# Kernel optimization log

Measured on AMD Instinct MI355X. Metric: run time of the kernel, lower is better.

## Reference

```python
import jax, jax.numpy as jnp
import numpy as np

# FlowNetC correlation config (kernel_size=1 -> pointwise patch; pad == max_displacement)
PAD = 20
MAX_DISP = 20
STRIDE2 = 2


def setup_inputs() -> dict:
    key = jax.random.key(0)
    k1, k2 = jax.random.split(key)
    B, C, H, W = 4, 256, 96, 96
    input1 = jax.random.normal(k1, (B, C, H, W), dtype=jnp.float32)
    input2 = jax.random.normal(k2, (B, C, H, W), dtype=jnp.float32)
    return {"input1": input1, "input2": input2}


def _correlation(x1, x2):
    # x1, x2: [B, C, H, W]. Output: [B, D*D, H, W] with D = 2*MAX_DISP//STRIDE2 + 1.
    B, C, H, W = x1.shape
    x2p = jnp.pad(x2, ((0, 0), (0, 0), (PAD, PAD), (PAD, PAD)))
    D = 2 * MAX_DISP // STRIDE2 + 1  # 21
    # start index into padded map = PAD + (disp) where disp = off - MAX_DISP;
    # since PAD == MAX_DISP, start index == off.
    offs = jnp.arange(D, dtype=jnp.int32) * STRIDE2
    dyv, dxv = jnp.meshgrid(offs, offs, indexing="ij")
    pairs = jnp.stack([dyv.ravel(), dxv.ravel()], axis=1)  # [D*D, 2]
    inv_c = jnp.float32(1.0 / C)  # CUDA kernel divides by kernel^2 * C (kernel=1)

    def body(_, p):
        dy, dx = p[0], p[1]
        sl = jax.lax.dynamic_slice(x2p, (0, 0, dy, dx), (B, C, H, W))
        return None, jnp.einsum("bchw,bchw->bhw", x1, sl) * inv_c

    _, corr = jax.lax.scan(body, None, pairs)  # [D*D, B, H, W]
    return corr.transpose(1, 0, 2, 3)  # [B, D*D, H, W]


def reference(input1, input2):
    return _correlation(input1, input2)
```

## Files before the change

### kernel.cpp

```cpp
#include <hip/hip_runtime.h>
#include <hip/hip_bf16.h>


typedef __bf16 bf16x8 __attribute__((ext_vector_type(8)));
typedef float f32x4 __attribute__((ext_vector_type(4)));

#define B_ 4
#define C_ 256
#define H_ 96
#define W_ 96
#define NOFF 21
#define ROWS 96
#define IMG_ELEMS (ROWS * C_)
#define X1T_ELEMS (B_ * H_ * IMG_ELEMS)

__device__ __forceinline__ unsigned short f32_to_bf16_rne(float f) {
    union { float f; unsigned u; } v; v.f = f;
    unsigned u = v.u;
    return (unsigned short)((u + 0x7fffu + ((u >> 16) & 1u)) >> 16);
}

__device__ __forceinline__ void gl2lds16(const void* g, void* l) {
    __builtin_amdgcn_global_load_lds(
        (const __attribute__((address_space(1))) void*)g,
        (__attribute__((address_space(3))) void*)l, 16, 0, 0);
}

__global__ __launch_bounds__(256) void prep_kernel(const float* __restrict__ x1,
                                                   const float* __restrict__ x2,
                                                   unsigned short* __restrict__ ws) {
    __shared__ float tile[96 * 65];
    int bid = blockIdx.x;
    int cblk  = bid & 3;
    int which = (bid >> 2) & 1;
    int bh    = bid >> 3;
    int h = bh % H_;
    int b = bh / H_;
    int c0 = cblk << 6;

    const float* src = (which ? x2 : x1) + ((size_t)(b * C_ + c0) * H_ + h) * W_;
    unsigned short* dst = ws + (size_t)which * X1T_ELEMS + (size_t)(b * H_ + h) * IMG_ELEMS;

    for (int idx = threadIdx.x; idx < 64 * 96; idx += 256) {
        int c = idx / 96, w = idx - c * 96;
        tile[w * 65 + c] = src[c * (H_ * W_) + w];
    }
    __syncthreads();

    for (int idx = threadIdx.x; idx < 96 * 8; idx += 256) {
        int row = idx >> 3, tp = idx & 7;
        int par = row / 48, i = row - par * 48;
        int w = 2 * i + par;
        int s = tp ^ (row & 7);
        const float* fsrc = &tile[w * 65 + (s << 3)];
        unsigned pk[4];
#pragma unroll
        for (int e = 0; e < 4; ++e) {
            unsigned lo = f32_to_bf16_rne(fsrc[2 * e]);
            unsigned hi = f32_to_bf16_rne(fsrc[2 * e + 1]);
            pk[e] = lo | (hi << 16);
        }
        int ccp = (((c0 >> 3) ^ (row & 24)) + tp);
        *(uint4*)((char*)(dst + (size_t)row * C_) + (ccp << 4)) =
            make_uint4(pk[0], pk[1], pk[2], pk[3]);
    }
}

__global__ __launch_bounds__(384, 3) void corr_kernel(const unsigned short* __restrict__ ws,
                                                      float* __restrict__ out) {
    __shared__ unsigned short Bs[IMG_ELEMS];
    __shared__ float sl[NOFF][97];

    int bid = blockIdx.x;
    int xcd = bid & 7, sidx = bid >> 3;
    int b  = xcd >> 1;
    int h  = ((xcd & 1) ? 48 : 0) + (sidx >> 1);
    int og = sidx & 1;

    int tid = threadIdx.x;
    int wv = tid >> 6, lane = tid & 63;
    int par = wv & 1, mt = wv >> 1;
    int i0 = mt << 4;
    int n = lane & 15, quad = lane >> 4;

    int rowA = par * 48 + i0 + n;
    const unsigned short* Ag = ws + (size_t)(b * H_ + h) * IMG_ELEMS + (size_t)rowA * C_;
    int keyA = rowA & 31;
    bf16x8 afrag[8];
#pragma unroll
    for (int ks = 0; ks < 8; ++ks)
        afrag[ks] = *(const bf16x8*)(Ag + ((((ks << 2) | quad) ^ keyA) << 3));

    const unsigned short* Bimg = ws + (size_t)X1T_ELEMS + (size_t)(b * H_) * IMG_ELEMS;

    int rowB0 = par * 48 + n;
    int rowB1 = rowB0 + 16;
    int rowB2 = rowB0 + 32;
    int keyB0 = rowB0 & 31, keyB1 = rowB1 & 31, keyB2 = rowB2 & 31;

    int oy_lo = og ? 11 : 0;
    int oy_hi = og ? NOFF : 11;
    int wvoff  = wv * 8192;
    int gmaoff = wvoff + lane * 16;

    for (int oy = oy_lo; oy < oy_hi; ++oy) {
        int h2 = h + 2 * oy - 20;
        int outb = ((b * 441 + oy * NOFF) * H_ + h) * W_;
        if (h2 < 0 || h2 >= H_) {
            for (int idx = tid; idx < NOFF * W_; idx += 384)
                out[outb + (idx / W_) * (H_ * W_) + (idx % W_)] = 0.0f;
            continue;
        }

        const char* Bg = (const char*)(Bimg + (size_t)h2 * IMG_ELEMS);
#pragma unroll
        for (int c = 0; c < 8; ++c)
            gl2lds16(Bg + gmaoff + c * 1024, (char*)Bs + wvoff + c * 1024);
        __syncthreads();

        f32x4 acc0 = {0.f,0.f,0.f,0.f}, acc1 = {0.f,0.f,0.f,0.f}, acc2 = {0.f,0.f,0.f,0.f};
        const char* Bsb = (const char*)Bs;
        if (mt == 0) {
#pragma unroll
            for (int ks = 0; ks < 8; ++ks) {
                int ci = (ks << 2) | quad;
                bf16x8 b0 = *(const bf16x8*)(Bsb + rowB0 * 512 + ((ci ^ keyB0) << 4));
                bf16x8 b1 = *(const bf16x8*)(Bsb + rowB1 * 512 + ((ci ^ keyB1) << 4));
                acc0 = __builtin_amdgcn_mfma_f32_16x16x32_bf16(afrag[ks], b0, acc0, 0, 0, 0);
                acc1 = __builtin_amdgcn_mfma_f32_16x16x32_bf16(afrag[ks], b1, acc1, 0, 0, 0);
            }
        } else if (mt == 1) {
#pragma unroll
            for (int ks = 0; ks < 8; ++ks) {
                int ci = (ks << 2) | quad;
                bf16x8 b0 = *(const bf16x8*)(Bsb + rowB0 * 512 + ((ci ^ keyB0) << 4));
                bf16x8 b1 = *(const bf16x8*)(Bsb + rowB1 * 512 + ((ci ^ keyB1) << 4));
                bf16x8 b2 = *(const bf16x8*)(Bsb + rowB2 * 512 + ((ci ^ keyB2) << 4));
                acc0 = __builtin_amdgcn_mfma_f32_16x16x32_bf16(afrag[ks], b0, acc0, 0, 0, 0);
                acc1 = __builtin_amdgcn_mfma_f32_16x16x32_bf16(afrag[ks], b1, acc1, 0, 0, 0);
                acc2 = __builtin_amdgcn_mfma_f32_16x16x32_bf16(afrag[ks], b2, acc2, 0, 0, 0);
            }
        } else {
#pragma unroll
            for (int ks = 0; ks < 8; ++ks) {
                int ci = (ks << 2) | quad;
                bf16x8 b1 = *(const bf16x8*)(Bsb + rowB1 * 512 + ((ci ^ keyB1) << 4));
                bf16x8 b2 = *(const bf16x8*)(Bsb + rowB2 * 512 + ((ci ^ keyB2) << 4));
                acc1 = __builtin_amdgcn_mfma_f32_16x16x32_bf16(afrag[ks], b1, acc1, 0, 0, 0);
                acc2 = __builtin_amdgcn_mfma_f32_16x16x32_bf16(afrag[ks], b2, acc2, 0, 0, 0);
            }
        }

#pragma unroll
        for (int r = 0; r < 4; ++r) {
            int m = (quad << 2) + r;
            int w = 2 * (i0 + m) + par;
            int oxb = n - i0 - m - 6;
            if (mt != 2) { int ox = 16 + oxb; if (ox >= 0 && ox < NOFF) sl[ox][w] = acc0[r]; }
            {             int ox = 32 + oxb; if (ox >= 0 && ox < NOFF) sl[ox][w] = acc1[r]; }
            if (mt != 0) { int ox = 48 + oxb; if (ox >= 0 && ox < NOFF) sl[ox][w] = acc2[r]; }
        }
        __syncthreads();

        for (int idx = tid; idx < NOFF * W_; idx += 384) {
            int ox = idx / W_, w = idx - ox * W_;
            int w2 = w + 2 * ox - 20;
            float v = (w2 >= 0 && w2 < W_) ? sl[ox][w] * (1.0f / 256.0f) : 0.0f;
            out[outb + ox * (H_ * W_) + w] = v;
        }
    }
}

__global__ __launch_bounds__(256) void corr_fallback(const float* __restrict__ x1,
                                                     const float* __restrict__ x2,
                                                     float* __restrict__ out) {
    int bid = blockIdx.x;
    int oy = bid % NOFF, h = (bid / NOFF) % H_, b = bid / (NOFF * H_);
    int dy = 2 * oy - 20, h2 = h + dy;
    int outbase = ((b * 441 + oy * NOFF) * H_ + h) * W_;
    for (int idx = threadIdx.x; idx < NOFF * W_; idx += 256) {
        int ox = idx / W_, w = idx % W_;
        float acc = 0.f;
        int w2 = w + 2 * ox - 20;
        if (h2 >= 0 && h2 < H_ && w2 >= 0 && w2 < W_) {
            const float* p1 = x1 + (size_t)b * C_ * H_ * W_ + h * W_ + w;
            const float* p2 = x2 + (size_t)b * C_ * H_ * W_ + h2 * W_ + w2;
            for (int c = 0; c < C_; ++c) acc += p1[c * (H_ * W_)] * p2[c * (H_ * W_)];
        }
        out[outbase + ox * (H_ * W_) + w] = acc * (1.0f / 256.0f);
    }
}

extern "C" void kernel_launch(void* const* d_in, const int* in_sizes, int n_in,
                              void* d_out, int out_size, void* d_ws, size_t ws_size,
                              hipStream_t stream) {
    const float* x1 = (const float*)d_in[0];
    const float* x2 = (const float*)d_in[1];
    float* out = (float*)d_out;

    size_t need = (size_t)2 * X1T_ELEMS * sizeof(unsigned short);
    if (ws_size >= need) {
        unsigned short* ws = (unsigned short*)d_ws;
        prep_kernel<<<B_ * H_ * 2 * 4, 256, 0, stream>>>(x1, x2, ws);
        corr_kernel<<<768, 384, 0, stream>>>(ws, out);
    } else {
        corr_fallback<<<B_ * H_ * NOFF, 256, 0, stream>>>(x1, x2, out);
    }
}
```

Baseline: 180.9 us.

## Triple-buffer B rows in LDS with async prefetch and counted waitcnt barriers

```diff
diff --git a/kernel.cpp b/kernel.cpp
--- a/kernel.cpp
+++ b/kernel.cpp
@@ -12,6 +12,7 @@
 #define NOFF 21
 #define ROWS 96
 #define IMG_ELEMS (ROWS * C_)
+#define IMG_BYTES (IMG_ELEMS * 2)
 #define X1T_ELEMS (B_ * H_ * IMG_ELEMS)
 
 __device__ __forceinline__ unsigned short f32_to_bf16_rne(float f) {
@@ -66,10 +67,11 @@
     }
 }
 
-__global__ __launch_bounds__(384, 3) void corr_kernel(const unsigned short* __restrict__ ws,
+__global__ __launch_bounds__(384, 1) void corr_kernel(const unsigned short* __restrict__ ws,
                                                       float* __restrict__ out) {
-    __shared__ unsigned short Bs[IMG_ELEMS];
+    __shared__ unsigned short Bs[3][IMG_ELEMS];
     __shared__ float sl[NOFF][97];
+    static_assert(sizeof(Bs) + sizeof(sl) <= 163840, "LDS budget");
 
     int bid = blockIdx.x;
     int xcd = bid & 7, sidx = bid >> 3;
@@ -100,26 +102,65 @@
 
     int oy_lo = og ? 11 : 0;
     int oy_hi = og ? NOFF : 11;
+
+    int vlo = oy_lo, vhi = oy_hi;
+    {
+        int lo = (h <= 20) ? ((21 - h) >> 1) : 0;
+        int hi = ((115 - h) >> 1) + 1;
+        if (lo > vlo) vlo = lo;
+        if (hi < vhi) vhi = hi;
+    }
+    int nv = vhi - vlo; if (nv < 0) nv = 0;
+
     int wvoff  = wv * 8192;
     int gmaoff = wvoff + lane * 16;
 
+    if (nv > 0) {
+        const char* Bg = (const char*)(Bimg + (size_t)(h + 2 * vlo - 20) * IMG_ELEMS);
+#pragma unroll
+        for (int c = 0; c < 8; ++c)
+            gl2lds16(Bg + gmaoff + c * 1024, (char*)Bs[0] + wvoff + c * 1024);
+    }
+    if (nv > 1) {
+        const char* Bg = (const char*)(Bimg + (size_t)(h + 2 * (vlo + 1) - 20) * IMG_ELEMS);
+#pragma unroll
+        for (int c = 0; c < 8; ++c)
+            gl2lds16(Bg + gmaoff + c * 1024, (char*)Bs[1] + wvoff + c * 1024);
+    }
+
     for (int oy = oy_lo; oy < oy_hi; ++oy) {
-        int h2 = h + 2 * oy - 20;
+        if (oy >= vlo && oy < vhi) continue;
         int outb = ((b * 441 + oy * NOFF) * H_ + h) * W_;
-        if (h2 < 0 || h2 >= H_) {
-            for (int idx = tid; idx < NOFF * W_; idx += 384)
-                out[outb + (idx / W_) * (H_ * W_) + (idx % W_)] = 0.0f;
-            continue;
-        }
-
-        const char* Bg = (const char*)(Bimg + (size_t)h2 * IMG_ELEMS);
-#pragma unroll
-        for (int c = 0; c < 8; ++c)
-            gl2lds16(Bg + gmaoff + c * 1024, (char*)Bs + wvoff + c * 1024);
-        __syncthreads();
+        for (int idx = tid; idx < NOFF * W_; idx += 384)
+            out[outb + (idx / W_) * (H_ * W_) + (idx % W_)] = 0.0f;
+    }
+
+    for (int k = 0; k < nv; ++k) {
+        int oy = vlo + k;
+        int cur = k % 3;
+
+        if (k + 2 < nv) {
+            int nb = (k + 2) % 3;
+            const char* Bg = (const char*)(Bimg + (size_t)(h + 2 * (oy + 2) - 20) * IMG_ELEMS);
+#pragma unroll
+            for (int c = 0; c < 8; ++c)
+                gl2lds16(Bg + gmaoff + c * 1024, (char*)Bs[nb] + wvoff + c * 1024);
+        }
+
+        if (k == 0) {
+            if (nv > 2)       asm volatile("s_waitcnt vmcnt(16)\ns_barrier" ::: "memory");
+            else if (nv == 2) asm volatile("s_waitcnt vmcnt(8)\ns_barrier" ::: "memory");
+            else              asm volatile("s_waitcnt vmcnt(0)\ns_barrier" ::: "memory");
+        } else if (k + 2 < nv) {
+            asm volatile("s_waitcnt vmcnt(21)\ns_barrier" ::: "memory");
+        } else if (k + 1 < nv) {
+            asm volatile("s_waitcnt vmcnt(13)\ns_barrier" ::: "memory");
+        } else {
+            asm volatile("s_waitcnt vmcnt(5)\ns_barrier" ::: "memory");
+        }
 
         f32x4 acc0 = {0.f,0.f,0.f,0.f}, acc1 = {0.f,0.f,0.f,0.f}, acc2 = {0.f,0.f,0.f,0.f};
-        const char* Bsb = (const char*)Bs;
+        const char* Bsb = (const char*)Bs[cur];
         if (mt == 0) {
 #pragma unroll
             for (int ks = 0; ks < 8; ++ks) {
@@ -160,8 +201,10 @@
             {             int ox = 32 + oxb; if (ox >= 0 && ox < NOFF) sl[ox][w] = acc1[r]; }
             if (mt != 0) { int ox = 48 + oxb; if (ox >= 0 && ox < NOFF) sl[ox][w] = acc2[r]; }
         }
-        __syncthreads();
-
+
+        asm volatile("s_waitcnt lgkmcnt(0)\ns_barrier" ::: "memory");
+
+        int outb = ((b * 441 + oy * NOFF) * H_ + h) * W_;
         for (int idx = tid; idx < NOFF * W_; idx += 384) {
             int ox = idx / W_, w = idx - ox * W_;
             int w2 = w + 2 * ox - 20;
```

Result: no change. 178.2 us (-1.5%).

## Share staged input2 rows across four output rows with double-buffered LDS pipeline

Applied to the files above, without the earlier changes.

```diff
diff --git a/kernel.cpp b/kernel.cpp
--- a/kernel.cpp
+++ b/kernel.cpp
@@ -12,6 +12,7 @@
 #define NOFF 21
 #define ROWS 96
 #define IMG_ELEMS (ROWS * C_)
+#define HALF_ELEMS (48 * C_)
 #define X1T_ELEMS (B_ * H_ * IMG_ELEMS)
 
 __device__ __forceinline__ unsigned short f32_to_bf16_rne(float f) {
@@ -66,109 +67,189 @@
     }
 }
 
-__global__ __launch_bounds__(384, 3) void corr_kernel(const unsigned short* __restrict__ ws,
+__global__ __launch_bounds__(192, 2) void corr_kernel(const unsigned short* __restrict__ ws,
                                                       float* __restrict__ out) {
-    __shared__ unsigned short Bs[IMG_ELEMS];
-    __shared__ float sl[NOFF][97];
+    __shared__ unsigned short Bs[2][HALF_ELEMS];
+    __shared__ float sl[4][NOFF][49];
+    static_assert(sizeof(Bs) + sizeof(sl) <= 81920, "need 2 blocks/CU");
 
     int bid = blockIdx.x;
     int xcd = bid & 7, sidx = bid >> 3;
     int b  = xcd >> 1;
-    int h  = ((xcd & 1) ? 48 : 0) + (sidx >> 1);
-    int og = sidx & 1;
+    int hh = xcd & 1;
+    int par = sidx & 1;
+    int t2  = sidx >> 1;
+    int og  = t2 & 3;
+    int qq  = t2 >> 2;
+    int gq = qq >> 1, ph = qq & 1;
+    int hA = 48 * hh + 8 * gq + ph;
+    int olo = (og * NOFF) >> 2;
+    int ohi = ((og + 1) * NOFF) >> 2;
 
     int tid = threadIdx.x;
     int wv = tid >> 6, lane = tid & 63;
-    int par = wv & 1, mt = wv >> 1;
+    int mt = wv;
     int i0 = mt << 4;
     int n = lane & 15, quad = lane >> 4;
 
+    int Loj[4], Hij[4];
+    int tlo = 1 << 30, thi = -(1 << 30);
+#pragma unroll
+    for (int j = 0; j < 4; ++j) {
+        int hj = hA + 2 * j;
+        int lo = (hj >= 21) ? 0 : ((21 - hj) >> 1);
+        int hi = ((115 - hj) >> 1) + 1;
+        if (lo < olo) lo = olo;
+        if (hi > ohi) hi = ohi;
+        Loj[j] = lo; Hij[j] = hi;
+        if (lo < hi) {
+            int a = lo + j, c = hi + j;
+            if (a < tlo) tlo = a;
+            if (c > thi) thi = c;
+        }
+    }
+    int nv = thi - tlo; if (nv < 0) nv = 0;
+
     int rowA = par * 48 + i0 + n;
-    const unsigned short* Ag = ws + (size_t)(b * H_ + h) * IMG_ELEMS + (size_t)rowA * C_;
     int keyA = rowA & 31;
-    bf16x8 afrag[8];
-#pragma unroll
-    for (int ks = 0; ks < 8; ++ks)
-        afrag[ks] = *(const bf16x8*)(Ag + ((((ks << 2) | quad) ^ keyA) << 3));
+    bf16x8 af[4][8];
+#pragma unroll
+    for (int pl = 0; pl < 4; ++pl) {
+        const unsigned short* Ag =
+            ws + (size_t)(b * H_ + hA + 2 * pl) * IMG_ELEMS + (size_t)rowA * C_;
+#pragma unroll
+        for (int ks = 0; ks < 8; ++ks)
+            af[pl][ks] = *(const bf16x8*)(Ag + ((((ks << 2) | quad) ^ keyA) << 3));
+    }
+    asm volatile("" ::: "memory");
+    __builtin_amdgcn_s_waitcnt(0);
 
     const unsigned short* Bimg = ws + (size_t)X1T_ELEMS + (size_t)(b * H_) * IMG_ELEMS;
 
-    int rowB0 = par * 48 + n;
-    int rowB1 = rowB0 + 16;
-    int rowB2 = rowB0 + 32;
-    int keyB0 = rowB0 & 31, keyB1 = rowB1 & 31, keyB2 = rowB2 & 31;
-
-    int oy_lo = og ? 11 : 0;
-    int oy_hi = og ? NOFF : 11;
     int wvoff  = wv * 8192;
     int gmaoff = wvoff + lane * 16;
 
-    for (int oy = oy_lo; oy < oy_hi; ++oy) {
-        int h2 = h + 2 * oy - 20;
-        int outb = ((b * 441 + oy * NOFF) * H_ + h) * W_;
-        if (h2 < 0 || h2 >= H_) {
-            for (int idx = tid; idx < NOFF * W_; idx += 384)
-                out[outb + (idx / W_) * (H_ * W_) + (idx % W_)] = 0.0f;
-            continue;
-        }
-
-        const char* Bg = (const char*)(Bimg + (size_t)h2 * IMG_ELEMS);
-#pragma unroll
-        for (int c = 0; c < 8; ++c)
-            gl2lds16(Bg + gmaoff + c * 1024, (char*)Bs + wvoff + c * 1024);
-        __syncthreads();
-
-        f32x4 acc0 = {0.f,0.f,0.f,0.f}, acc1 = {0.f,0.f,0.f,0.f}, acc2 = {0.f,0.f,0.f,0.f};
-        const char* Bsb = (const char*)Bs;
-        if (mt == 0) {
-#pragma unroll
-            for (int ks = 0; ks < 8; ++ks) {
-                int ci = (ks << 2) | quad;
-                bf16x8 b0 = *(const bf16x8*)(Bsb + rowB0 * 512 + ((ci ^ keyB0) << 4));
-                bf16x8 b1 = *(const bf16x8*)(Bsb + rowB1 * 512 + ((ci ^ keyB1) << 4));
-                acc0 = __builtin_amdgcn_mfma_f32_16x16x32_bf16(afrag[ks], b0, acc0, 0, 0, 0);
-                acc1 = __builtin_amdgcn_mfma_f32_16x16x32_bf16(afrag[ks], b1, acc1, 0, 0, 0);
+#define STAGE(slot, tt) do {                                                          \
+    const char* Bg_ = (const char*)(Bimg + (size_t)(hA + 2 * (tt) - 20) * IMG_ELEMS   \
+                                    + par * HALF_ELEMS);                              \
+    _Pragma("unroll")                                                                 \
+    for (int c = 0; c < 8; ++c)                                                       \
+        gl2lds16(Bg_ + gmaoff + c * 1024, (char*)Bs[slot] + wvoff + c * 1024);        \
+} while (0)
+
+    if (nv > 0) STAGE(0, tlo);
+    if (nv > 1) STAGE(1, tlo + 1);
+    asm volatile("" ::: "memory");
+
+#pragma unroll
+    for (int pl = 0; pl < 4; ++pl) {
+        int hp = hA + 2 * pl;
+        for (int oy = olo; oy < ohi; ++oy) {
+            if (oy >= Loj[pl] && oy < Hij[pl]) continue;
+            int outb = ((b * 441 + oy * NOFF) * H_ + hp) * W_;
+#pragma unroll
+            for (int jj = 0; jj < 6; ++jj) {
+                int idx = tid + jj * 192;
+                if (idx < NOFF * 48) {
+                    int ox = idx / 48, i = idx - ox * 48;
+                    out[outb + ox * (H_ * W_) + 2 * i + par] = 0.0f;
+                }
             }
-        } else if (mt == 1) {
-#pragma unroll
-            for (int ks = 0; ks < 8; ++ks) {
-                int ci = (ks << 2) | quad;
-                bf16x8 b0 = *(const bf16x8*)(Bsb + rowB0 * 512 + ((ci ^ keyB0) << 4));
-                bf16x8 b1 = *(const bf16x8*)(Bsb + rowB1 * 512 + ((ci ^ keyB1) << 4));
-                bf16x8 b2 = *(const bf16x8*)(Bsb + rowB2 * 512 + ((ci ^ keyB2) << 4));
-                acc0 = __builtin_amdgcn_mfma_f32_16x16x32_bf16(afrag[ks], b0, acc0, 0, 0, 0);
-                acc1 = __builtin_amdgcn_mfma_f32_16x16x32_bf16(afrag[ks], b1, acc1, 0, 0, 0);
-                acc2 = __builtin_amdgcn_mfma_f32_16x16x32_bf16(afrag[ks], b2, acc2, 0, 0, 0);
-            }
+        }
+    }
+
+    int locB[3] = { n, n + 16, n + 32 };
+    int keyB[3] = { (n + 16 * par) & 31,
+                    (n + 16 + 16 * par) & 31,
+                    (n + 32 + 16 * par) & 31 };
+    bool useu[3] = { mt != 2, true, mt != 0 };
+
+    for (int k = 0; k < nv; ++k) {
+        int t = tlo + k;
+        int cur = k & 1;
+
+        if (k == 0) {
+            if (nv > 1) asm volatile("s_waitcnt vmcnt(8)\ns_barrier" ::: "memory");
+            else        asm volatile("s_waitcnt vmcnt(0)\ns_barrier" ::: "memory");
+        } else if (k == 1) {
+            if (nv > 2) asm volatile("s_waitcnt vmcnt(13)\ns_barrier" ::: "memory");
+            else        asm volatile("s_waitcnt vmcnt(5)\ns_barrier" ::: "memory");
+        } else if (k + 1 == nv) {
+            asm volatile("s_waitcnt vmcnt(10)\ns_barrier" ::: "memory");
         } else {
-#pragma unroll
-            for (int ks = 0; ks < 8; ++ks) {
-                int ci = (ks << 2) | quad;
-                bf16x8 b1 = *(const bf16x8*)(Bsb + rowB1 * 512 + ((ci ^ keyB1) << 4));
-                bf16x8 b2 = *(const bf16x8*)(Bsb + rowB2 * 512 + ((ci ^ keyB2) << 4));
-                acc1 = __builtin_amdgcn_mfma_f32_16x16x32_bf16(afrag[ks], b1, acc1, 0, 0, 0);
-                acc2 = __builtin_amdgcn_mfma_f32_16x16x32_bf16(afrag[ks], b2, acc2, 0, 0, 0);
-            }
-        }
+            asm volatile("s_waitcnt vmcnt(18)\ns_barrier" ::: "memory");
+        }
+
+        const char* Bsb = (const char*)Bs[cur];
+        f32x4 acc[4][3];
+#pragma unroll
+        for (int pl = 0; pl < 4; ++pl)
+#pragma unroll
+            for (int u = 0; u < 3; ++u)
+                acc[pl][u] = (f32x4){0.f, 0.f, 0.f, 0.f};
+
+        __builtin_amdgcn_s_setprio(1);
+#pragma unroll
+        for (int ks = 0; ks < 8; ++ks) {
+            int ci = (ks << 2) | quad;
+            bf16x8 bfr[3];
+#pragma unroll
+            for (int u = 0; u < 3; ++u)
+                if (useu[u])
+                    bfr[u] = *(const bf16x8*)(Bsb + locB[u] * 512 + ((ci ^ keyB[u]) << 4));
+#pragma unroll
+            for (int u = 0; u < 3; ++u)
+                if (useu[u]) {
+#pragma unroll
+                    for (int pl = 0; pl < 4; ++pl)
+                        acc[pl][u] = __builtin_amdgcn_mfma_f32_16x16x32_bf16(
+                            af[pl][ks], bfr[u], acc[pl][u], 0, 0, 0);
+                }
+        }
+        __builtin_amdgcn_s_setprio(0);
 
 #pragma unroll
         for (int r = 0; r < 4; ++r) {
             int m = (quad << 2) + r;
-            int w = 2 * (i0 + m) + par;
-            int oxb = n - i0 - m - 6;
-            if (mt != 2) { int ox = 16 + oxb; if (ox >= 0 && ox < NOFF) sl[ox][w] = acc0[r]; }
-            {             int ox = 32 + oxb; if (ox >= 0 && ox < NOFF) sl[ox][w] = acc1[r]; }
-            if (mt != 0) { int ox = 48 + oxb; if (ox >= 0 && ox < NOFF) sl[ox][w] = acc2[r]; }
-        }
-        __syncthreads();
-
-        for (int idx = tid; idx < NOFF * W_; idx += 384) {
-            int ox = idx / W_, w = idx - ox * W_;
-            int w2 = w + 2 * ox - 20;
-            float v = (w2 >= 0 && w2 < W_) ? sl[ox][w] * (1.0f / 256.0f) : 0.0f;
-            out[outb + ox * (H_ * W_) + w] = v;
-        }
-    }
+            int io = i0 + m;
+            int oxb = n - io - 6;
+#pragma unroll
+            for (int u = 0; u < 3; ++u) {
+                if (!useu[u]) continue;
+                int ox = 16 * (u + 1) + oxb;
+                if (ox >= 0 && ox < NOFF) {
+#pragma unroll
+                    for (int pl = 0; pl < 4; ++pl)
+                        sl[pl][ox][io] = acc[pl][u][r];
+                }
+            }
+        }
+
+        asm volatile("s_waitcnt lgkmcnt(0)\ns_barrier" ::: "memory");
+
+        if (k + 2 < nv) STAGE(cur, t + 2);
+        asm volatile("" ::: "memory");
+
+#pragma unroll
+        for (int pl = 0; pl < 4; ++pl) {
+            int oyp = t - pl;
+            if (oyp < Loj[pl] || oyp >= Hij[pl]) continue;
+            int hp = hA + 2 * pl;
+            int outb = ((b * 441 + oyp * NOFF) * H_ + hp) * W_;
+#pragma unroll
+            for (int jj = 0; jj < 6; ++jj) {
+                int idx = tid + jj * 192;
+                if (idx < NOFF * 48) {
+                    int ox = idx / 48, i = idx - ox * 48;
+                    int w = 2 * i + par;
+                    int w2 = w + 2 * ox - 20;
+                    float v = (w2 >= 0 && w2 < W_) ? sl[pl][ox][i] * (1.0f / 256.0f) : 0.0f;
+                    out[outb + ox * (H_ * W_) + w] = v;
+                }
+            }
+        }
+    }
+#undef STAGE
 }
 
 __global__ __launch_bounds__(256) void corr_fallback(const float* __restrict__ x1,
@@ -202,7 +283,7 @@
     if (ws_size >= need) {
         unsigned short* ws = (unsigned short*)d_ws;
         prep_kernel<<<B_ * H_ * 2 * 4, 256, 0, stream>>>(x1, x2, ws);
-        corr_kernel<<<768, 384, 0, stream>>>(ws, out);
+        corr_kernel<<<768, 192, 0, stream>>>(ws, out);
     } else {
         corr_fallback<<<B_ * H_ * NOFF, 256, 0, stream>>>(x1, x2, out);
     }
```

Measured after the change: 175.7 us. 2.9% less time.
